# Performance work log

Measured on AMD Instinct MI355X. Metric: run time of the kernel, lower is better.

The kernel has to match this reference:

```python
import jax, jax.numpy as jnp
import numpy as np

N_NODES = 100000
N_GRAPHS = 64

def gcn_conv(x, edge_index, W, b, num_nodes):
    # PyG GCNConv: x' = D^-1/2 (A + I) D^-1/2 (x W) + b
    h = x @ W  # [N, out]
    row, col = edge_index[0], edge_index[1]
    loops = jnp.arange(num_nodes, dtype=row.dtype)
    src = jnp.concatenate([row, loops])  # message source (x_j)
    dst = jnp.concatenate([col, loops])  # aggregation target
    deg = jax.ops.segment_sum(jnp.ones_like(src, dtype=h.dtype), dst,
                              num_segments=num_nodes)
    dinv = jnp.where(deg > 0, jax.lax.rsqrt(deg), 0.0)
    norm = dinv[src] * dinv[dst]  # [E+N]
    msgs = h[src] * norm[:, None]  # gather-transform
    out = jax.ops.segment_sum(msgs, dst, num_segments=num_nodes)  # scatter
    return out + b

def global_mean_pool(x, batch, num_graphs):
    sums = jax.ops.segment_sum(x, batch, num_segments=num_graphs)
    cnts = jax.ops.segment_sum(jnp.ones((x.shape[0],), x.dtype), batch,
                               num_segments=num_graphs)
    return sums / jnp.maximum(cnts, 1.0)[:, None]

def setup_inputs() -> dict:
    key = jax.random.key(0)
    ks = jax.random.split(key, 12)
    d_in, d_hid, d_mid, d_out = 128, 128, 20, 10
    n_edges = 1600000
    x = jax.random.normal(ks[0], (N_NODES, d_in), dtype=jnp.float32)
    edge_index = jax.random.randint(ks[1], (2, n_edges), 0, N_NODES, dtype=jnp.int64)
    batch = jnp.sort(jax.random.randint(ks[2], (N_NODES,), 0, N_GRAPHS, dtype=jnp.int64))
    def glorot(k, fan_in, fan_out):
        s = (6.0 / (fan_in + fan_out)) ** 0.5
        return jax.random.uniform(k, (fan_in, fan_out), jnp.float32, -s, s)
    return {
        "x": x, "edge_index": edge_index, "batch": batch,
        "W1": glorot(ks[3], d_in, d_hid), "b1": jnp.zeros((d_hid,), jnp.float32),
        "W2": glorot(ks[4], d_hid, d_hid), "b2": jnp.zeros((d_hid,), jnp.float32),
        "fc1_W": glorot(ks[5], d_hid, d_mid), "fc1_b": jnp.zeros((d_mid,), jnp.float32),
        "fc2_W": glorot(ks[6], d_mid, d_out), "fc2_b": jnp.zeros((d_out,), jnp.float32),
    }

def reference(x, edge_index, batch, W1, b1, W2, b2, fc1_W, fc1_b, fc2_W, fc2_b):
    # eval mode: dropout is identity
    h = gcn_conv(x, edge_index, W1, b1, N_NODES)
    h = jax.nn.elu(h)
    h = gcn_conv(h, edge_index, W2, b2, N_NODES)
    g = global_mean_pool(h, batch, N_GRAPHS)  # [G, hidden]
    g = jax.nn.relu(g @ fc1_W + fc1_b)
    g = g @ fc2_W + fc2_b
    return jax.nn.log_softmax(g, axis=1)
```

## Files before the change

kernel.cpp:

```cpp
#include <hip/hip_runtime.h>
#include <math.h>

#define DH 128
#define BCAP 16384

typedef __bf16 bf8_t __attribute__((ext_vector_type(8)));
typedef short short8 __attribute__((ext_vector_type(8)));
typedef float f4_t __attribute__((ext_vector_type(4)));
typedef float f2_t __attribute__((ext_vector_type(2)));

__device__ inline unsigned short f2b(float f) {
    unsigned int u = __builtin_bit_cast(unsigned int, f);
    u = u + 0x7fffu + ((u >> 16) & 1u);
    return (unsigned short)(u >> 16);
}
__device__ inline float b2f(unsigned short h) {
    return __builtin_bit_cast(float, (unsigned int)h << 16);
}

__global__ __launch_bounds__(256) void k_bucket(const int* __restrict__ row,
                                                const int* __restrict__ col,
                                                int E, int nbuck, int chunk,
                                                unsigned int* __restrict__ pairs,
                                                int* __restrict__ bcur) {
    __shared__ int lcnt[256];
    __shared__ int lbase[256];
    __shared__ unsigned int srec[8192];
    int t = threadIdx.x;
    int e0 = blockIdx.x * chunk;
    int e1 = min(e0 + chunk, E);
    lcnt[t] = 0;
    __syncthreads();
    for (int i = e0 + t; i < e1; i += 256) {
        int d = col[i];
        int b = d >> 9;
        int slot = atomicAdd(&lcnt[b], 1);
        srec[i - e0] = ((unsigned int)b << 22) | ((unsigned int)(d & 511) << 13)
                     | (unsigned int)slot;
    }
    __syncthreads();
    if (t < nbuck) {
        int c = lcnt[t];
        lbase[t] = (c > 0) ? atomicAdd(&bcur[t * 16], c) : 0;
    }
    __syncthreads();
    for (int i = e0 + t; i < e1; i += 256) {
        unsigned int r = srec[i - e0];
        int b = r >> 22;
        unsigned int dl = (r >> 13) & 511u;
        int slot = (int)(r & 8191u);
        int g = lbase[b] + slot;
        if (g < BCAP)
            pairs[(size_t)b * BCAP + g] = ((unsigned int)row[i] << 9) | dl;
    }
}

__global__ __launch_bounds__(256) void k_build(const unsigned int* __restrict__ pairs,
                                               const int* __restrict__ bcur,
                                               int nbuck, int N,
                                               int* __restrict__ off,
                                               int* __restrict__ dpd,
                                               float* __restrict__ dinv,
                                               int* __restrict__ csr) {
    __shared__ int cnt2[512];
    __shared__ int pd2[512];
    __shared__ int excl[512];
    __shared__ int curi[512];
    __shared__ int stmp[256];
    int b = blockIdx.x, t = threadIdx.x;
    int cnt = min(bcur[b * 16], BCAP);
    int base = b * BCAP;
    int node0 = b << 9;
    int nodes = min(512, N - node0);
    cnt2[t] = (t < nodes) ? 1 : 0;
    cnt2[t + 256] = (t + 256 < nodes) ? 1 : 0;
    __syncthreads();
    const unsigned int* pp = pairs + (size_t)b * BCAP;
    for (int i = t; i < cnt; i += 256)
        atomicAdd(&cnt2[pp[i] & 511u], 1);
    __syncthreads();
    pd2[t] = (cnt2[t] + 15) & ~15;
    pd2[t + 256] = (cnt2[t + 256] + 15) & ~15;
    __syncthreads();
    stmp[t] = pd2[2 * t] + pd2[2 * t + 1];
    __syncthreads();
    for (int d = 1; d < 256; d <<= 1) {
        int v = (t >= d) ? stmp[t - d] : 0;
        __syncthreads();
        stmp[t] += v;
        __syncthreads();
    }
    int pre = (t == 0) ? 0 : stmp[t - 1];
    excl[2 * t] = pre;
    excl[2 * t + 1] = pre + pd2[2 * t];
    __syncthreads();
    for (int n = t; n < 512; n += 256) {
        int avail = BCAP - excl[n];
        int pdc = pd2[n];
        if (pdc > avail) pdc = (avail > 0) ? (avail & ~15) : 0;
        pd2[n] = pdc;
    }
    __syncthreads();
    if (t < nodes) {
        off[node0 + t] = base + excl[t];
        dpd[node0 + t] = pd2[t];
        dinv[node0 + t] = rsqrtf((float)cnt2[t]);
    }
    int t2 = t + 256;
    if (t2 < nodes) {
        off[node0 + t2] = base + excl[t2];
        dpd[node0 + t2] = pd2[t2];
        dinv[node0 + t2] = rsqrtf((float)cnt2[t2]);
    }
    curi[t] = excl[t] + 1; curi[t + 256] = excl[t + 256] + 1;
    __syncthreads();
    for (int n = t; n < nodes; n += 256)
        if (excl[n] < BCAP) csr[base + excl[n]] = node0 + n;
    for (int i = t; i < cnt; i += 256) {
        unsigned int p = pp[i];
        int d = (int)(p & 511u);
        int slot = atomicAdd(&curi[d], 1);
        if (slot < BCAP) csr[base + slot] = (int)(p >> 9);
    }
    for (int n = t; n < 512; n += 256) {
        int e0 = excl[n] + cnt2[n];
        int e1 = excl[n] + pd2[n];
        for (int k = e0; k < e1; k++) csr[base + k] = N;
    }
}

__global__ void k_prepW(const float* __restrict__ W1, const float* __restrict__ W2,
                        unsigned short* __restrict__ Wt1, unsigned short* __restrict__ Wt2) {
    int t = blockIdx.x * blockDim.x + threadIdx.x;
    int v = t & 16383;
    int k = v >> 7, n = v & 127;
    if (t < 16384) {
        Wt1[n * DH + k] = f2b(W1[k * DH + n]);
    } else {
        int p = ((k & 15) << 3) | (k >> 4);
        Wt2[n * DH + p] = f2b(W2[k * DH + n]);
    }
}

__global__ __launch_bounds__(256) void k_gemm_mfma(const void* __restrict__ Xin, int x_is_bf16,
                                                   const unsigned short* __restrict__ Wt,
                                                   const float* __restrict__ dinv,
                                                   unsigned char* __restrict__ Y, int nrows) {
    __shared__ unsigned short Xs[64 * 136];
    __shared__ unsigned short Ws[128 * 136];
    int t = threadIdx.x;
    int row0 = blockIdx.x * 64;

    for (int v = t; v < 128 * 32; v += 256) {
        int n = v >> 5, kq = v & 31;
        ushort4 w = ((const ushort4*)Wt)[v];
        *(ushort4*)&Ws[n * 136 + kq * 4] = w;
    }
    if (x_is_bf16) {
        const unsigned short* X = (const unsigned short*)Xin;
        for (int v = t; v < 64 * 32; v += 256) {
            int r = v >> 5, cq = v & 31;
            int gr = row0 + r;
            ushort4 h;
            if (gr < nrows) h = ((const ushort4*)X)[(size_t)gr * 32 + cq];
            else { h.x = 0; h.y = 0; h.z = 0; h.w = 0; }
            *(ushort4*)&Xs[r * 136 + cq * 4] = h;
        }
    } else {
        const float* X = (const float*)Xin;
        for (int v = t; v < 64 * 32; v += 256) {
            int r = v >> 5, cq = v & 31;
            int gr = row0 + r;
            ushort4 h;
            if (gr < nrows) {
                float4 xv = ((const float4*)X)[(size_t)gr * 32 + cq];
                h.x = f2b(xv.x); h.y = f2b(xv.y); h.z = f2b(xv.z); h.w = f2b(xv.w);
            } else { h.x = 0; h.y = 0; h.z = 0; h.w = 0; }
            *(ushort4*)&Xs[r * 136 + cq * 4] = h;
        }
    }
    __syncthreads();

    int w = t >> 6;
    int lane = t & 63;
    int quad = lane >> 4;
    int l16 = lane & 15;
    int rw = w * 16;

    f4_t acc[8];
#pragma unroll
    for (int j = 0; j < 8; j++) acc[j] = (f4_t){0.f, 0.f, 0.f, 0.f};

#pragma unroll
    for (int kk = 0; kk < 4; kk++) {
        int k0 = kk * 32;
        bf8_t a = __builtin_bit_cast(bf8_t,
            *(const short8*)&Xs[(rw + l16) * 136 + k0 + quad * 8]);
#pragma unroll
        for (int j = 0; j < 8; j++) {
            bf8_t b = __builtin_bit_cast(bf8_t,
                *(const short8*)&Ws[(j * 16 + l16) * 136 + k0 + quad * 8]);
            acc[j] = __builtin_amdgcn_mfma_f32_16x16x32_bf16(a, b, acc[j], 0, 0, 0);
        }
    }

#pragma unroll
    for (int reg = 0; reg < 4; reg++) {
        int r = row0 + rw + quad * 4 + reg;
        if (r < nrows) {
            float dv = dinv[r];
            float v0 = acc[0][reg] * dv, v1 = acc[1][reg] * dv;
            float v2 = acc[2][reg] * dv, v3 = acc[3][reg] * dv;
            float v4 = acc[4][reg] * dv, v5 = acc[5][reg] * dv;
            float v6 = acc[6][reg] * dv, v7 = acc[7][reg] * dv;
            int d0 = __builtin_amdgcn_cvt_pk_fp8_f32(v0, v1, 0, false);
            d0 = __builtin_amdgcn_cvt_pk_fp8_f32(v2, v3, d0, true);
            int d1 = __builtin_amdgcn_cvt_pk_fp8_f32(v4, v5, 0, false);
            d1 = __builtin_amdgcn_cvt_pk_fp8_f32(v6, v7, d1, true);
            *(uint2*)&Y[(size_t)r * DH + l16 * 8] = make_uint2((unsigned)d0, (unsigned)d1);
        }
    }
}

#define AGG_ROUND(IDX)                                                     \
    {                                                                      \
        int ea = be + i;                                                   \
        unsigned v0 = ((unsigned)IDX(ea)     << 7) | l5b;                  \
        unsigned v1 = ((unsigned)IDX(ea + 1) << 7) | l5b;                  \
        unsigned v2 = ((unsigned)IDX(ea + 2) << 7) | l5b;                  \
        unsigned v3 = ((unsigned)IDX(ea + 3) << 7) | l5b;                  \
        unsigned v4 = ((unsigned)IDX(ea + 4) << 7) | l5b;                  \
        unsigned v5 = ((unsigned)IDX(ea + 5) << 7) | l5b;                  \
        unsigned v6 = ((unsigned)IDX(ea + 6) << 7) | l5b;                  \
        unsigned v7 = ((unsigned)IDX(ea + 7) << 7) | l5b;                  \
        unsigned int u0 = *(const unsigned int*)(Tb + v0);                 \
        unsigned int u1 = *(const unsigned int*)(Tb + v1);                 \
        unsigned int u2 = *(const unsigned int*)(Tb + v2);                 \
        unsigned int u3 = *(const unsigned int*)(Tb + v3);                 \
        unsigned int u4 = *(const unsigned int*)(Tb + v4);                 \
        unsigned int u5 = *(const unsigned int*)(Tb + v5);                 \
        unsigned int u6 = *(const unsigned int*)(Tb + v6);                 \
        unsigned int u7 = *(const unsigned int*)(Tb + v7);                 \
        accA01 += __builtin_amdgcn_cvt_pk_f32_fp8(u0, false);              \
        accA23 += __builtin_amdgcn_cvt_pk_f32_fp8(u0, true);               \
        accB01 += __builtin_amdgcn_cvt_pk_f32_fp8(u1, false);              \
        accB23 += __builtin_amdgcn_cvt_pk_f32_fp8(u1, true);               \
        accA01 += __builtin_amdgcn_cvt_pk_f32_fp8(u2, false);              \
        accA23 += __builtin_amdgcn_cvt_pk_f32_fp8(u2, true);               \
        accB01 += __builtin_amdgcn_cvt_pk_f32_fp8(u3, false);              \
        accB23 += __builtin_amdgcn_cvt_pk_f32_fp8(u3, true);               \
        accA01 += __builtin_amdgcn_cvt_pk_f32_fp8(u4, false);              \
        accA23 += __builtin_amdgcn_cvt_pk_f32_fp8(u4, true);               \
        accB01 += __builtin_amdgcn_cvt_pk_f32_fp8(u5, false);              \
        accB23 += __builtin_amdgcn_cvt_pk_f32_fp8(u5, true);               \
        accA01 += __builtin_amdgcn_cvt_pk_f32_fp8(u6, false);              \
        accA23 += __builtin_amdgcn_cvt_pk_f32_fp8(u6, true);               \
        accB01 += __builtin_amdgcn_cvt_pk_f32_fp8(u7, false);              \
        accB23 += __builtin_amdgcn_cvt_pk_f32_fp8(u7, true);               \
    }

__global__ __launch_bounds__(256) void k_agg(const unsigned char* __restrict__ T,
                                             unsigned short* __restrict__ Out,
                                             const float* __restrict__ dinv,
                                             const int* __restrict__ off,
                                             const int* __restrict__ dpd,
                                             const int* __restrict__ csr,
                                             const float* __restrict__ bias,
                                             int elu, int N) {
    __shared__ int ofs[16];
    __shared__ int pds[16];
    __shared__ float dv16[16];
    __shared__ int sidx[768];
    int t = threadIdx.x;
    int d0 = blockIdx.x * 16;
    if (t < 16) {
        int n = min(d0 + t, N - 1);
        ofs[t] = off[n];
        pds[t] = dpd[n];
        dv16[t] = dinv[n];
    }
    __syncthreads();
    int s0 = ofs[0];
    int span = ofs[15] + pds[15] - s0;
    int scnt = min(span, 768);
    for (int k = t; k < scnt; k += 256) sidx[k] = csr[s0 + k];
    __syncthreads();

    int w = t >> 6;
    int lane = t & 63;
    int half = lane >> 5;
    int l5 = lane & 31;
    unsigned l5b = (unsigned)(l5 << 2);
    const char* Tb = (const char*)T;

    int c0 = ((l5 & 1) << 6) | (l5 >> 1);
    float bb0 = bias[c0], bb1 = bias[c0 + 16], bb2 = bias[c0 + 32], bb3 = bias[c0 + 48];

    for (int ni = 0; ni < 4; ni++) {
        int nl = 4 * w + ni;
        int nd = d0 + nl;
        if (nd >= N) break;
        int eL = ofs[nl] - s0;
        int pd = pds[nl];
        int K = pd >> 1;
        int be = eL + half * K;

        f2_t accA01 = (f2_t){0.f, 0.f}, accA23 = (f2_t){0.f, 0.f};
        f2_t accB01 = (f2_t){0.f, 0.f}, accB23 = (f2_t){0.f, 0.f};

        if (eL + pd <= scnt) {
#define IDX_L(e) sidx[e]
            for (int i = 0; i < K; i += 8) AGG_ROUND(IDX_L)
#undef IDX_L
        } else {
            const int* gp = csr + s0;
#define IDX_G(e) gp[e]
            for (int i = 0; i < K; i += 8) AGG_ROUND(IDX_G)
#undef IDX_G
        }

        float a0 = accA01[0] + accB01[0];
        float a1 = accA01[1] + accB01[1];
        float a2 = accA23[0] + accB23[0];
        float a3 = accA23[1] + accB23[1];
        a0 += __shfl_xor(a0, 32);
        a1 += __shfl_xor(a1, 32);
        a2 += __shfl_xor(a2, 32);
        a3 += __shfl_xor(a3, 32);

        if (!half) {
            float dv = dv16[nl];
            float o0 = a0 * dv + bb0;
            float o1 = a1 * dv + bb1;
            float o2 = a2 * dv + bb2;
            float o3 = a3 * dv + bb3;
            if (elu) {
                o0 = o0 > 0.f ? o0 : __expf(o0) - 1.f;
                o1 = o1 > 0.f ? o1 : __expf(o1) - 1.f;
                o2 = o2 > 0.f ? o2 : __expf(o2) - 1.f;
                o3 = o3 > 0.f ? o3 : __expf(o3) - 1.f;
            }
            unsigned int p0 = (unsigned int)f2b(o0) | ((unsigned int)f2b(o1) << 16);
            unsigned int p1 = (unsigned int)f2b(o2) | ((unsigned int)f2b(o3) << 16);
            *(uint2*)&Out[(size_t)nd * DH + (l5 << 2)] = make_uint2(p0, p1);
        }
    }
}

__global__ __launch_bounds__(256) void k_pool(const unsigned int* __restrict__ H32,
                                              const int* __restrict__ batch,
                                              float* __restrict__ Gsum,
                                              int* __restrict__ cnts, int N) {
    int g = blockIdx.x;
    int p = blockIdx.y;
    int t = threadIdx.x;
    int lane = t & 63;
    int rg = t >> 6;
    int lo = 0, hi = N;
    while (lo < hi) { int m = (lo + hi) >> 1; if (batch[m] < g) lo = m + 1; else hi = m; }
    int s = lo;
    hi = N;
    while (lo < hi) { int m = (lo + hi) >> 1; if (batch[m] < g + 1) lo = m + 1; else hi = m; }
    int e = lo;
    int len = e - s;
    int parts = (int)gridDim.y;
    int chunk = (len + parts - 1) / parts;
    int i0 = s + p * chunk;
    int i1 = min(i0 + chunk, e);
    float a0 = 0.f, a1 = 0.f;
    for (int i = i0 + rg; i < i1; i += 4) {
        unsigned int v = H32[(size_t)i * 64 + lane];
        a0 += b2f((unsigned short)(v & 0xffffu));
        a1 += b2f((unsigned short)(v >> 16));
    }
    __shared__ float ps[4][DH];
    ps[rg][lane * 2] = a0;
    ps[rg][lane * 2 + 1] = a1;
    __syncthreads();
    if (t < DH) {
        float v = ps[0][t] + ps[1][t] + ps[2][t] + ps[3][t];
        atomicAdd(&Gsum[g * DH + t], v);
    }
    if (p == 0 && t == 0) cnts[g] = len;
}

__global__ __launch_bounds__(64) void k_head(const float* __restrict__ Gsum,
                                             const int* __restrict__ cnts,
                                             const float* __restrict__ W1,
                                             const float* __restrict__ b1,
                                             const float* __restrict__ W2,
                                             const float* __restrict__ b2,
                                             float* __restrict__ out) {
    int g = blockIdx.x;
    int t = threadIdx.x;
    __shared__ float gv[DH];
    __shared__ float mid[20];
    __shared__ float o[10];
    float inv = 1.f / fmaxf((float)cnts[g], 1.f);
    for (int i = t; i < DH; i += 64) {
        int c = ((i & 7) << 4) | (i >> 3);
        gv[c] = Gsum[g * DH + i] * inv;
    }
    __syncthreads();
    if (t < 20) {
        float a = b1[t];
        for (int k = 0; k < DH; k++) a += gv[k] * W1[k * 20 + t];
        mid[t] = fmaxf(a, 0.f);
    }
    __syncthreads();
    if (t < 10) {
        float a = b2[t];
        for (int k = 0; k < 20; k++) a += mid[k] * W2[k * 10 + t];
        o[t] = a;
    }
    __syncthreads();
    if (t == 0) {
        float m = -1e30f;
        for (int j = 0; j < 10; j++) m = fmaxf(m, o[j]);
        float ssum = 0.f;
        for (int j = 0; j < 10; j++) ssum += expf(o[j] - m);
        float l = logf(ssum);
        for (int j = 0; j < 10; j++) out[g * 10 + j] = o[j] - m - l;
    }
}

extern "C" void kernel_launch(void* const* d_in, const int* in_sizes, int n_in,
                              void* d_out, int out_size, void* d_ws, size_t ws_size,
                              hipStream_t stream) {
    const float* x    = (const float*)d_in[0];
    const int*   ei   = (const int*)d_in[1];
    const int*   batch= (const int*)d_in[2];
    const float* W1   = (const float*)d_in[3];
    const float* b1   = (const float*)d_in[4];
    const float* W2   = (const float*)d_in[5];
    const float* b2   = (const float*)d_in[6];
    const float* fc1W = (const float*)d_in[7];
    const float* fc1b = (const float*)d_in[8];
    const float* fc2W = (const float*)d_in[9];
    const float* fc2b = (const float*)d_in[10];
    float* out = (float*)d_out;

    int N = in_sizes[0] / DH;
    int E = in_sizes[1] / 2;
    int G = out_size / 10;
    int nbuck = (N + 511) >> 9;

    char* p = (char*)d_ws;
    auto alloc = [&](size_t bytes) {
        char* r = p;
        p += (bytes + 255) & ~(size_t)255;
        return r;
    };
    size_t pairs_bytes = (size_t)nbuck * BCAP * 4;
    size_t t8_bytes = (size_t)(N + 1) * DH;
    char* region = alloc(pairs_bytes > t8_bytes ? pairs_bytes : t8_bytes);
    unsigned int*   pairs = (unsigned int*)region;
    unsigned char*  t8    = (unsigned char*)region;
    unsigned short* a1 = (unsigned short*)alloc((size_t)N * DH * 2);
    int*   csr  = (int*)alloc((size_t)nbuck * BCAP * 4);
    int*   off  = (int*)alloc((size_t)N * 4);
    int*   dpd  = (int*)alloc((size_t)N * 4);
    float* dinv = (float*)alloc((size_t)N * 4);
    unsigned short* Wt1 = (unsigned short*)alloc(DH * DH * 2);
    unsigned short* Wt2 = (unsigned short*)alloc(DH * DH * 2);
    float* Gsum = (float*)alloc((size_t)G * DH * 4);
    int*   bcur = (int*)alloc(256 * 16 * 4);
    int*   cnts = (int*)alloc((size_t)G * 4);

    const int* row = ei;
    const int* col = ei + E;

    (void)hipMemsetAsync(Gsum, 0, (size_t)G * DH * 4 + 256 * 16 * 4, stream);

    const int chunk = 8192;
    int ablocks = (E + chunk - 1) / chunk;
    k_bucket<<<ablocks, 256, 0, stream>>>(row, col, E, nbuck, chunk, pairs, bcur);
    k_build<<<nbuck, 256, 0, stream>>>(pairs, bcur, nbuck, N, off, dpd, dinv, csr);
    (void)hipMemsetAsync(t8 + (size_t)N * DH, 0, DH, stream);
    k_prepW<<<128, 256, 0, stream>>>(W1, W2, Wt1, Wt2);

    int gblocks = (N + 63) / 64;
    int mblocks = (N + 15) / 16;
    k_gemm_mfma<<<gblocks, 256, 0, stream>>>(x, 0, Wt1, dinv, t8, N);
    k_agg<<<mblocks, 256, 0, stream>>>(t8, a1, dinv, off, dpd, csr, b1, 1, N);
    k_gemm_mfma<<<gblocks, 256, 0, stream>>>(a1, 1, Wt2, dinv, t8, N);
    k_agg<<<mblocks, 256, 0, stream>>>(t8, a1, dinv, off, dpd, csr, b2, 0, N);

    dim3 pg(G, 32);
    k_pool<<<pg, 256, 0, stream>>>((const unsigned int*)a1, batch, Gsum, cnts, N);
    k_head<<<G, 64, 0, stream>>>(Gsum, cnts, fc1W, fc1b, fc2W, fc2b, out);
}
```

Before: 298.4 us.

## Fuse second GCN aggregation with global mean pooling via shared-memory atomics

The second aggregation kernel now accumulates each node's output directly into per-graph sums in shared memory and flushes them to global memory with atomics. This removes the separate pooling kernel and the write and re-read of the full bf16 hidden activation. Graph node counts are now computed in the head kernel by binary search, and the zero-row memset is folded into the weight-prep kernel to drop a launch. The cost is atomic traffic on shared and global memory, and Gacc adds 8 KB of shared memory per block, which may lower occupancy.

```diff
diff --git a/kernel.cpp b/kernel.cpp
--- a/kernel.cpp
+++ b/kernel.cpp
@@ -130,8 +130,10 @@
 }
 
 __global__ void k_prepW(const float* __restrict__ W1, const float* __restrict__ W2,
-                        unsigned short* __restrict__ Wt1, unsigned short* __restrict__ Wt2) {
+                        unsigned short* __restrict__ Wt1, unsigned short* __restrict__ Wt2,
+                        unsigned int* __restrict__ t8zrow) {
     int t = blockIdx.x * blockDim.x + threadIdx.x;
+    if (blockIdx.x == 0 && threadIdx.x < 32) t8zrow[threadIdx.x] = 0u;
     int v = t & 16383;
     int k = v >> 7, n = v & 127;
     if (t < 16384) {
@@ -266,7 +268,7 @@
                                              const int* __restrict__ dpd,
                                              const int* __restrict__ csr,
                                              const float* __restrict__ bias,
-                                             int elu, int N) {
+                                             int N) {
     __shared__ int ofs[16];
     __shared__ int pds[16];
     __shared__ float dv16[16];
@@ -334,12 +336,10 @@
             float o1 = a1 * dv + bb1;
             float o2 = a2 * dv + bb2;
             float o3 = a3 * dv + bb3;
-            if (elu) {
-                o0 = o0 > 0.f ? o0 : __expf(o0) - 1.f;
-                o1 = o1 > 0.f ? o1 : __expf(o1) - 1.f;
-                o2 = o2 > 0.f ? o2 : __expf(o2) - 1.f;
-                o3 = o3 > 0.f ? o3 : __expf(o3) - 1.f;
-            }
+            o0 = o0 > 0.f ? o0 : __expf(o0) - 1.f;
+            o1 = o1 > 0.f ? o1 : __expf(o1) - 1.f;
+            o2 = o2 > 0.f ? o2 : __expf(o2) - 1.f;
+            o3 = o3 > 0.f ? o3 : __expf(o3) - 1.f;
             unsigned int p0 = (unsigned int)f2b(o0) | ((unsigned int)f2b(o1) << 16);
             unsigned int p1 = (unsigned int)f2b(o2) | ((unsigned int)f2b(o3) << 16);
             *(uint2*)&Out[(size_t)nd * DH + (l5 << 2)] = make_uint2(p0, p1);
@@ -347,45 +347,100 @@
     }
 }
 
-__global__ __launch_bounds__(256) void k_pool(const unsigned int* __restrict__ H32,
+__global__ __launch_bounds__(256) void k_aggp(const unsigned char* __restrict__ T,
+                                              float* __restrict__ Gsum,
+                                              const float* __restrict__ dinv,
+                                              const int* __restrict__ off,
+                                              const int* __restrict__ dpd,
+                                              const int* __restrict__ csr,
+                                              const float* __restrict__ bias,
                                               const int* __restrict__ batch,
-                                              float* __restrict__ Gsum,
-                                              int* __restrict__ cnts, int N) {
-    int g = blockIdx.x;
-    int p = blockIdx.y;
+                                              int N) {
+    __shared__ int ofs[16];
+    __shared__ int pds[16];
+    __shared__ float dv16[16];
+    __shared__ int gfs[16];
+    __shared__ int sidx[768];
+    __shared__ float Gacc[16 * DH];
     int t = threadIdx.x;
+    int d0 = blockIdx.x * 16;
+    if (t < 16) {
+        int n = min(d0 + t, N - 1);
+        ofs[t] = off[n];
+        pds[t] = dpd[n];
+        dv16[t] = dinv[n];
+        gfs[t] = batch[n];
+    }
+    for (int k = t; k < 16 * DH; k += 256) Gacc[k] = 0.f;
+    __syncthreads();
+    int s0 = ofs[0];
+    int g0 = gfs[0];
+    int span = ofs[15] + pds[15] - s0;
+    int scnt = min(span, 768);
+    for (int k = t; k < scnt; k += 256) sidx[k] = csr[s0 + k];
+    __syncthreads();
+
+    int w = t >> 6;
     int lane = t & 63;
-    int rg = t >> 6;
-    int lo = 0, hi = N;
-    while (lo < hi) { int m = (lo + hi) >> 1; if (batch[m] < g) lo = m + 1; else hi = m; }
-    int s = lo;
-    hi = N;
-    while (lo < hi) { int m = (lo + hi) >> 1; if (batch[m] < g + 1) lo = m + 1; else hi = m; }
-    int e = lo;
-    int len = e - s;
-    int parts = (int)gridDim.y;
-    int chunk = (len + parts - 1) / parts;
-    int i0 = s + p * chunk;
-    int i1 = min(i0 + chunk, e);
-    float a0 = 0.f, a1 = 0.f;
-    for (int i = i0 + rg; i < i1; i += 4) {
-        unsigned int v = H32[(size_t)i * 64 + lane];
-        a0 += b2f((unsigned short)(v & 0xffffu));
-        a1 += b2f((unsigned short)(v >> 16));
-    }
-    __shared__ float ps[4][DH];
-    ps[rg][lane * 2] = a0;
-    ps[rg][lane * 2 + 1] = a1;
-    __syncthreads();
-    if (t < DH) {
-        float v = ps[0][t] + ps[1][t] + ps[2][t] + ps[3][t];
-        atomicAdd(&Gsum[g * DH + t], v);
-    }
-    if (p == 0 && t == 0) cnts[g] = len;
+    int half = lane >> 5;
+    int l5 = lane & 31;
+    unsigned l5b = (unsigned)(l5 << 2);
+    const char* Tb = (const char*)T;
+
+    int c0 = ((l5 & 1) << 6) | (l5 >> 1);
+    float bb0 = bias[c0], bb1 = bias[c0 + 16], bb2 = bias[c0 + 32], bb3 = bias[c0 + 48];
+
+    for (int ni = 0; ni < 4; ni++) {
+        int nl = 4 * w + ni;
+        int nd = d0 + nl;
+        if (nd >= N) break;
+        int eL = ofs[nl] - s0;
+        int pd = pds[nl];
+        int K = pd >> 1;
+        int be = eL + half * K;
+
+        f2_t accA01 = (f2_t){0.f, 0.f}, accA23 = (f2_t){0.f, 0.f};
+        f2_t accB01 = (f2_t){0.f, 0.f}, accB23 = (f2_t){0.f, 0.f};
+
+        if (eL + pd <= scnt) {
+#define IDX_L(e) sidx[e]
+            for (int i = 0; i < K; i += 8) AGG_ROUND(IDX_L)
+#undef IDX_L
+        } else {
+            const int* gp = csr + s0;
+#define IDX_G(e) gp[e]
+            for (int i = 0; i < K; i += 8) AGG_ROUND(IDX_G)
+#undef IDX_G
+        }
+
+        float a0 = accA01[0] + accB01[0];
+        float a1 = accA01[1] + accB01[1];
+        float a2 = accA23[0] + accB23[0];
+        float a3 = accA23[1] + accB23[1];
+        a0 += __shfl_xor(a0, 32);
+        a1 += __shfl_xor(a1, 32);
+        a2 += __shfl_xor(a2, 32);
+        a3 += __shfl_xor(a3, 32);
+
+        if (!half) {
+            float dv = dv16[nl];
+            int sbase = (gfs[nl] - g0) * DH;
+            atomicAdd(&Gacc[sbase + c0],      a0 * dv + bb0);
+            atomicAdd(&Gacc[sbase + c0 + 16], a1 * dv + bb1);
+            atomicAdd(&Gacc[sbase + c0 + 32], a2 * dv + bb2);
+            atomicAdd(&Gacc[sbase + c0 + 48], a3 * dv + bb3);
+        }
+    }
+    __syncthreads();
+    int nspan = gfs[15] - g0 + 1;
+    for (int k = t; k < nspan * DH; k += 256) {
+        float v = Gacc[k];
+        if (v != 0.f) atomicAdd(&Gsum[(size_t)(g0 + (k >> 7)) * DH + (k & 127)], v);
+    }
 }
 
 __global__ __launch_bounds__(64) void k_head(const float* __restrict__ Gsum,
-                                             const int* __restrict__ cnts,
+                                             const int* __restrict__ batch, int N,
                                              const float* __restrict__ W1,
                                              const float* __restrict__ b1,
                                              const float* __restrict__ W2,
@@ -396,11 +451,13 @@
     __shared__ float gv[DH];
     __shared__ float mid[20];
     __shared__ float o[10];
-    float inv = 1.f / fmaxf((float)cnts[g], 1.f);
-    for (int i = t; i < DH; i += 64) {
-        int c = ((i & 7) << 4) | (i >> 3);
-        gv[c] = Gsum[g * DH + i] * inv;
-    }
+    int lo = 0, hi = N;
+    while (lo < hi) { int m = (lo + hi) >> 1; if (batch[m] < g) lo = m + 1; else hi = m; }
+    int s = lo;
+    hi = N;
+    while (lo < hi) { int m = (lo + hi) >> 1; if (batch[m] < g + 1) lo = m + 1; else hi = m; }
+    float inv = 1.f / fmaxf((float)(lo - s), 1.f);
+    for (int i = t; i < DH; i += 64) gv[i] = Gsum[g * DH + i] * inv;
     __syncthreads();
     if (t < 20) {
         float a = b1[t];
@@ -465,7 +522,6 @@
     unsigned short* Wt2 = (unsigned short*)alloc(DH * DH * 2);
     float* Gsum = (float*)alloc((size_t)G * DH * 4);
     int*   bcur = (int*)alloc(256 * 16 * 4);
-    int*   cnts = (int*)alloc((size_t)G * 4);
 
     const int* row = ei;
     const int* col = ei + E;
@@ -476,17 +532,15 @@
     int ablocks = (E + chunk - 1) / chunk;
     k_bucket<<<ablocks, 256, 0, stream>>>(row, col, E, nbuck, chunk, pairs, bcur);
     k_build<<<nbuck, 256, 0, stream>>>(pairs, bcur, nbuck, N, off, dpd, dinv, csr);
-    (void)hipMemsetAsync(t8 + (size_t)N * DH, 0, DH, stream);
-    k_prepW<<<128, 256, 0, stream>>>(W1, W2, Wt1, Wt2);
+    k_prepW<<<128, 256, 0, stream>>>(W1, W2, Wt1, Wt2,
+                                     (unsigned int*)(t8 + (size_t)N * DH));
 
     int gblocks = (N + 63) / 64;
     int mblocks = (N + 15) / 16;
     k_gemm_mfma<<<gblocks, 256, 0, stream>>>(x, 0, Wt1, dinv, t8, N);
-    k_agg<<<mblocks, 256, 0, stream>>>(t8, a1, dinv, off, dpd, csr, b1, 1, N);
+    k_agg<<<mblocks, 256, 0, stream>>>(t8, a1, dinv, off, dpd, csr, b1, N);
     k_gemm_mfma<<<gblocks, 256, 0, stream>>>(a1, 1, Wt2, dinv, t8, N);
-    k_agg<<<mblocks, 256, 0, stream>>>(t8, a1, dinv, off, dpd, csr, b2, 0, N);
-
-    dim3 pg(G, 32);
-    k_pool<<<pg, 256, 0, stream>>>((const unsigned int*)a1, batch, Gsum, cnts, N);
-    k_head<<<G, 64, 0, stream>>>(Gsum, cnts, fc1W, fc1b, fc2W, fc2b, out);
-}
+    k_aggp<<<mblocks, 256, 0, stream>>>(t8, Gsum, dinv, off, dpd, csr, b2, batch, N);
+
+    k_head<<<G, 64, 0, stream>>>(Gsum, batch, N, fc1W, fc1b, fc2W, fc2b, out);
+}
```

New measurement: 335.2 us. 1.12x slower.

## Split CSR build into scan kernel plus grid-parallel scatter, shrink bucket chunks

Applied to the files above, without the earlier changes.

The CSR construction is restructured so each bucket block only counts degrees and computes offsets with 512 threads. The per-edge scatter moves to a separate kernel that spreads each bucket across 8 blocks and uses global atomic cursors. The bucketing chunk is cut from 8192 to 2048 edges, which means more blocks and less shared memory per block. A memset is folded into the weight-prep kernel. The aim is more parallelism in the preprocessing stage, at the cost of an extra launch and contended global atomics.

```diff
diff --git a/kernel.cpp b/kernel.cpp
--- a/kernel.cpp
+++ b/kernel.cpp
@@ -25,7 +25,7 @@
                                                 int* __restrict__ bcur) {
     __shared__ int lcnt[256];
     __shared__ int lbase[256];
-    __shared__ unsigned int srec[8192];
+    __shared__ unsigned int srec[2048];
     int t = threadIdx.x;
     int e0 = blockIdx.x * chunk;
     int e1 = min(e0 + chunk, E);
@@ -55,83 +55,74 @@
     }
 }
 
-__global__ __launch_bounds__(256) void k_build(const unsigned int* __restrict__ pairs,
+__global__ __launch_bounds__(512) void k_build(const unsigned int* __restrict__ pairs,
                                                const int* __restrict__ bcur,
                                                int nbuck, int N,
                                                int* __restrict__ off,
                                                int* __restrict__ dpd,
                                                float* __restrict__ dinv,
-                                               int* __restrict__ csr) {
+                                               int* __restrict__ csr,
+                                               int* __restrict__ gcur) {
     __shared__ int cnt2[512];
-    __shared__ int pd2[512];
-    __shared__ int excl[512];
-    __shared__ int curi[512];
-    __shared__ int stmp[256];
+    __shared__ int scn[512];
     int b = blockIdx.x, t = threadIdx.x;
     int cnt = min(bcur[b * 16], BCAP);
     int base = b * BCAP;
     int node0 = b << 9;
     int nodes = min(512, N - node0);
     cnt2[t] = (t < nodes) ? 1 : 0;
-    cnt2[t + 256] = (t + 256 < nodes) ? 1 : 0;
     __syncthreads();
     const unsigned int* pp = pairs + (size_t)b * BCAP;
-    for (int i = t; i < cnt; i += 256)
+    for (int i = t; i < cnt; i += 512)
         atomicAdd(&cnt2[pp[i] & 511u], 1);
     __syncthreads();
-    pd2[t] = (cnt2[t] + 15) & ~15;
-    pd2[t + 256] = (cnt2[t + 256] + 15) & ~15;
-    __syncthreads();
-    stmp[t] = pd2[2 * t] + pd2[2 * t + 1];
-    __syncthreads();
-    for (int d = 1; d < 256; d <<= 1) {
-        int v = (t >= d) ? stmp[t - d] : 0;
+    int c = cnt2[t];
+    int pdv = (c + 15) & ~15;
+    scn[t] = pdv;
+    __syncthreads();
+    for (int d = 1; d < 512; d <<= 1) {
+        int v = (t >= d) ? scn[t - d] : 0;
         __syncthreads();
-        stmp[t] += v;
+        scn[t] += v;
         __syncthreads();
     }
-    int pre = (t == 0) ? 0 : stmp[t - 1];
-    excl[2 * t] = pre;
-    excl[2 * t + 1] = pre + pd2[2 * t];
-    __syncthreads();
-    for (int n = t; n < 512; n += 256) {
-        int avail = BCAP - excl[n];
-        int pdc = pd2[n];
-        if (pdc > avail) pdc = (avail > 0) ? (avail & ~15) : 0;
-        pd2[n] = pdc;
-    }
-    __syncthreads();
+    int excl = scn[t] - pdv;
+    int exc = min(excl, BCAP);
+    int avail = BCAP - exc;
+    int pdc = min(pdv, avail);
     if (t < nodes) {
-        off[node0 + t] = base + excl[t];
-        dpd[node0 + t] = pd2[t];
-        dinv[node0 + t] = rsqrtf((float)cnt2[t]);
-    }
-    int t2 = t + 256;
-    if (t2 < nodes) {
-        off[node0 + t2] = base + excl[t2];
-        dpd[node0 + t2] = pd2[t2];
-        dinv[node0 + t2] = rsqrtf((float)cnt2[t2]);
-    }
-    curi[t] = excl[t] + 1; curi[t + 256] = excl[t + 256] + 1;
-    __syncthreads();
-    for (int n = t; n < nodes; n += 256)
-        if (excl[n] < BCAP) csr[base + excl[n]] = node0 + n;
-    for (int i = t; i < cnt; i += 256) {
+        off[node0 + t] = base + exc;
+        dpd[node0 + t] = pdc;
+        dinv[node0 + t] = rsqrtf((float)c);
+        gcur[node0 + t] = base + exc + 1;
+        if (pdc > 0) csr[base + exc] = node0 + t;
+        for (int k = c; k < pdc; k++) csr[base + exc + k] = N;
+    }
+}
+
+__global__ __launch_bounds__(256) void k_scatter(const unsigned int* __restrict__ pairs,
+                                                 const int* __restrict__ bcur,
+                                                 int* __restrict__ gcur,
+                                                 int* __restrict__ csr) {
+    int b = blockIdx.x;
+    int cnt = min(bcur[b * 16], BCAP);
+    int node0 = b << 9;
+    int hi = b * BCAP + BCAP;
+    const unsigned int* pp = pairs + (size_t)b * BCAP;
+    int stride = (int)gridDim.y * 256;
+    for (int i = blockIdx.y * 256 + threadIdx.x; i < cnt; i += stride) {
         unsigned int p = pp[i];
         int d = (int)(p & 511u);
-        int slot = atomicAdd(&curi[d], 1);
-        if (slot < BCAP) csr[base + slot] = (int)(p >> 9);
-    }
-    for (int n = t; n < 512; n += 256) {
-        int e0 = excl[n] + cnt2[n];
-        int e1 = excl[n] + pd2[n];
-        for (int k = e0; k < e1; k++) csr[base + k] = N;
+        int slot = atomicAdd(&gcur[node0 + d], 1);
+        if (slot < hi) csr[slot] = (int)(p >> 9);
     }
 }
 
 __global__ void k_prepW(const float* __restrict__ W1, const float* __restrict__ W2,
-                        unsigned short* __restrict__ Wt1, unsigned short* __restrict__ Wt2) {
+                        unsigned short* __restrict__ Wt1, unsigned short* __restrict__ Wt2,
+                        unsigned int* __restrict__ t8zrow) {
     int t = blockIdx.x * blockDim.x + threadIdx.x;
+    if (blockIdx.x == 0 && threadIdx.x < 32) t8zrow[threadIdx.x] = 0u;
     int v = t & 16383;
     int k = v >> 7, n = v & 127;
     if (t < 16384) {
@@ -461,6 +452,7 @@
     int*   off  = (int*)alloc((size_t)N * 4);
     int*   dpd  = (int*)alloc((size_t)N * 4);
     float* dinv = (float*)alloc((size_t)N * 4);
+    int*   gcur = (int*)alloc((size_t)N * 4);
     unsigned short* Wt1 = (unsigned short*)alloc(DH * DH * 2);
     unsigned short* Wt2 = (unsigned short*)alloc(DH * DH * 2);
     float* Gsum = (float*)alloc((size_t)G * DH * 4);
@@ -472,12 +464,13 @@
 
     (void)hipMemsetAsync(Gsum, 0, (size_t)G * DH * 4 + 256 * 16 * 4, stream);
 
-    const int chunk = 8192;
+    const int chunk = 2048;
     int ablocks = (E + chunk - 1) / chunk;
     k_bucket<<<ablocks, 256, 0, stream>>>(row, col, E, nbuck, chunk, pairs, bcur);
-    k_build<<<nbuck, 256, 0, stream>>>(pairs, bcur, nbuck, N, off, dpd, dinv, csr);
-    (void)hipMemsetAsync(t8 + (size_t)N * DH, 0, DH, stream);
-    k_prepW<<<128, 256, 0, stream>>>(W1, W2, Wt1, Wt2);
+    k_build<<<nbuck, 512, 0, stream>>>(pairs, bcur, nbuck, N, off, dpd, dinv, csr, gcur);
+    k_scatter<<<dim3(nbuck, 8), 256, 0, stream>>>(pairs, bcur, gcur, csr);
+    k_prepW<<<128, 256, 0, stream>>>(W1, W2, Wt1, Wt2,
+                                     (unsigned int*)(t8 + (size_t)N * DH));
 
     int gblocks = (N + 63) / 64;
     int mblocks = (N + 15) / 16;
```

After: 322.5 us. 1.08x slower.
